# Optimization experiments

Hardware: AMD Instinct MI355X
Metric: run time of the kernel (lower is better)

The kernel has to match this reference:

```python
import jax, jax.numpy as jnp
import numpy as np

N = 100001      # item_num + 1
D = 64          # hidden_units
NNZ = 3200000   # number of nonzeros in encoder_adj (avg degree ~32)


def setup_inputs() -> dict:
    key = jax.random.key(0)
    k1, k2, k3, k4 = jax.random.split(key, 4)
    row_idx = jax.random.randint(k1, (NNZ,), 0, N, dtype=jnp.int32)
    col_idx = jax.random.randint(k2, (NNZ,), 0, N, dtype=jnp.int32)
    adj_vals = jax.random.uniform(k3, (NNZ,), dtype=jnp.float32)
    emb_weight = jax.random.normal(k4, (N, D), dtype=jnp.float32)
    return {"row_idx": row_idx, "col_idx": col_idx, "adj_vals": adj_vals,
            "emb_weight": emb_weight}


def _spmm(row_idx, col_idx, vals, x):
    # COO SpMM: out[r] += vals[e] * x[col[e]]  -> [N, D]
    gathered = vals[:, None] * x[col_idx]          # [NNZ, D]
    return jax.ops.segment_sum(gathered, row_idx, num_segments=N)


def reference(row_idx, col_idx, adj_vals, emb_weight):
    e0 = emb_weight                                 # ego embeddings
    e1 = _spmm(row_idx, col_idx, adj_vals, e0)      # GCN layer 1
    e2 = _spmm(row_idx, col_idx, adj_vals, e1)      # GCN layer 2
    summed = e0 + e1 + e2                           # sum(embeds)
    return (summed, e0, e1, e2)
```

## Files before the change

kernel.cpp:

```cpp
#include <hip/hip_runtime.h>
#include <stdint.h>

#define DHID 64
#define G_BLOCKS 1024
#define BMAX 1024
#define RPB 128

static inline size_t align256(size_t x) { return (x + 255) & ~(size_t)255; }


__global__ void zero_f32(float* __restrict__ p, size_t n) {
  size_t i = (size_t)blockIdx.x * blockDim.x + threadIdx.x;
  if (i < n) p[i] = 0.f;
}


__global__ __launch_bounds__(256) void
a1_hist_k(const int* __restrict__ row, int* __restrict__ histGB,
          int nnz, int B, int chunk) {
  __shared__ int h[BMAX];
  for (int i = threadIdx.x; i < B; i += 256) h[i] = 0;
  __syncthreads();
  int g = blockIdx.x;
  int s = g * chunk, e = min(nnz, s + chunk);
  int j = s + threadIdx.x;
  for (; j + 768 < e; j += 1024) {
    int r0 = row[j], r1 = row[j + 256], r2 = row[j + 512], r3 = row[j + 768];
    atomicAdd(&h[r0 >> 7], 1);
    atomicAdd(&h[r1 >> 7], 1);
    atomicAdd(&h[r2 >> 7], 1);
    atomicAdd(&h[r3 >> 7], 1);
  }
  for (; j < e; j += 256)
    atomicAdd(&h[row[j] >> 7], 1);
  __syncthreads();
  for (int i = threadIdx.x; i < B; i += 256)
    histGB[i * G_BLOCKS + g] = h[i];
}

__global__ __launch_bounds__(256) void
scan_gb_k(const int* __restrict__ histGB, int* __restrict__ offGB,
          int* __restrict__ btot, int B) {
  __shared__ int wsum[4];
  int b = blockIdx.x, t = threadIdx.x, lane = t & 63, w = t >> 6;
  int v[4];
  int s4 = 0;
#pragma unroll
  for (int i = 0; i < 4; ++i) {
    v[i] = histGB[b * G_BLOCKS + t * 4 + i];
    s4 += v[i];
  }
  int incl = s4;
#pragma unroll
  for (int off = 1; off < 64; off <<= 1) {
    int u = __shfl_up(incl, off);
    if (lane >= off) incl += u;
  }
  if (lane == 63) wsum[w] = incl;
  __syncthreads();
  int run = incl - s4;
  for (int w2 = 0; w2 < w; ++w2) run += wsum[w2];
#pragma unroll
  for (int i = 0; i < 4; ++i) {
    offGB[b * G_BLOCKS + t * 4 + i] = run;
    run += v[i];
  }
  if (t == 0) btot[b] = wsum[0] + wsum[1] + wsum[2] + wsum[3];
}

__global__ void scan_b_k(const int* __restrict__ btot, int* __restrict__ base, int B) {
  __shared__ int wsum[4];
  int t = threadIdx.x, lane = t & 63, w = t >> 6;
  int v[8];
  int s = 0;
#pragma unroll
  for (int i = 0; i < 8; ++i) {
    int idx = t * 8 + i;
    v[i] = (idx < B) ? btot[idx] : 0;
    s += v[i];
  }
  int incl = s;
#pragma unroll
  for (int off = 1; off < 64; off <<= 1) {
    int u = __shfl_up(incl, off);
    if (lane >= off) incl += u;
  }
  if (lane == 63) wsum[w] = incl;
  __syncthreads();
  int run = incl - s;
  for (int w2 = 0; w2 < w; ++w2) run += wsum[w2];
#pragma unroll
  for (int i = 0; i < 8; ++i) {
    int idx = t * 8 + i;
    if (idx <= B) base[idx] = run;
    run += v[i];
  }
}

__global__ __launch_bounds__(256) void
a2_scatter_k(const int* __restrict__ row, const int* __restrict__ col,
             const float* __restrict__ val, const int* __restrict__ base,
             const int* __restrict__ offGB, int2* __restrict__ stage,
             int nnz, int B, int chunk) {
  __shared__ int cur[BMAX];
  int g = blockIdx.x;
  for (int i = threadIdx.x; i < B; i += 256)
    cur[i] = base[i] + offGB[i * G_BLOCKS + g];
  __syncthreads();
  int s = g * chunk, e = min(nnz, s + chunk);
  int j = s + threadIdx.x;
  for (; j + 768 < e; j += 1024) {
    int r0 = row[j], r1 = row[j + 256], r2 = row[j + 512], r3 = row[j + 768];
    int c0 = col[j], c1 = col[j + 256], c2 = col[j + 512], c3 = col[j + 768];
    float v0 = val[j], v1 = val[j + 256], v2 = val[j + 512], v3 = val[j + 768];
    int p0 = atomicAdd(&cur[r0 >> 7], 1);
    int p1 = atomicAdd(&cur[r1 >> 7], 1);
    int p2 = atomicAdd(&cur[r2 >> 7], 1);
    int p3 = atomicAdd(&cur[r3 >> 7], 1);
    int2 q0; q0.x = ((r0 & 127) << 24) | c0; q0.y = __float_as_int(v0);
    int2 q1; q1.x = ((r1 & 127) << 24) | c1; q1.y = __float_as_int(v1);
    int2 q2; q2.x = ((r2 & 127) << 24) | c2; q2.y = __float_as_int(v2);
    int2 q3; q3.x = ((r3 & 127) << 24) | c3; q3.y = __float_as_int(v3);
    stage[p0] = q0;
    stage[p1] = q1;
    stage[p2] = q2;
    stage[p3] = q3;
  }
  for (; j < e; j += 256) {
    int r = row[j];
    int pos = atomicAdd(&cur[r >> 7], 1);
    int2 p;
    p.x = ((r & 127) << 24) | col[j];
    p.y = __float_as_int(val[j]);
    stage[pos] = p;
  }
}


__global__ __launch_bounds__(256) void
bgroup_k(const int* __restrict__ base, const int2* __restrict__ stage,
         int2* __restrict__ edges, int* __restrict__ rowstart, int n, int nnz) {
  __shared__ int h[RPB];
  __shared__ int cur[RPB];
  __shared__ int w0sum;
  int b = blockIdx.x, t = threadIdx.x;
  int lane = t & 63, w = t >> 6;
  if (t < RPB) h[t] = 0;
  __syncthreads();
  int s = base[b], e = base[b + 1];
  {
    int j = s + t;
    for (; j + 768 < e; j += 1024) {
      int a0 = ((unsigned)stage[j].x) >> 24;
      int a1 = ((unsigned)stage[j + 256].x) >> 24;
      int a2 = ((unsigned)stage[j + 512].x) >> 24;
      int a3 = ((unsigned)stage[j + 768].x) >> 24;
      atomicAdd(&h[a0], 1);
      atomicAdd(&h[a1], 1);
      atomicAdd(&h[a2], 1);
      atomicAdd(&h[a3], 1);
    }
    for (; j < e; j += 256)
      atomicAdd(&h[((unsigned)stage[j].x) >> 24], 1);
  }
  __syncthreads();
  int v = 0, incl = 0;
  if (t < RPB) {
    v = h[t];
    incl = v;
#pragma unroll
    for (int off = 1; off < 64; off <<= 1) {
      int u = __shfl_up(incl, off);
      if (lane >= off) incl += u;
    }
    if (t == 63) w0sum = incl;
  }
  __syncthreads();
  if (t < RPB) {
    int excl = incl - v + ((w == 1) ? w0sum : 0);
    cur[t] = s + excl;
    int r = (b << 7) + t;
    if (r < n) rowstart[r] = s + excl;
  }
  if (b == 0 && t == 0) rowstart[n] = nnz;
  __syncthreads();
  {
    int j = s + t;
    for (; j + 768 < e; j += 1024) {
      int2 p0 = stage[j], p1 = stage[j + 256], p2 = stage[j + 512], p3 = stage[j + 768];
      int q0 = atomicAdd(&cur[((unsigned)p0.x) >> 24], 1);
      int q1 = atomicAdd(&cur[((unsigned)p1.x) >> 24], 1);
      int q2 = atomicAdd(&cur[((unsigned)p2.x) >> 24], 1);
      int q3 = atomicAdd(&cur[((unsigned)p3.x) >> 24], 1);
      int2 o0; o0.x = p0.x & 0xFFFFFF; o0.y = p0.y;
      int2 o1; o1.x = p1.x & 0xFFFFFF; o1.y = p1.y;
      int2 o2; o2.x = p2.x & 0xFFFFFF; o2.y = p2.y;
      int2 o3; o3.x = p3.x & 0xFFFFFF; o3.y = p3.y;
      edges[q0] = o0;
      edges[q1] = o1;
      edges[q2] = o2;
      edges[q3] = o3;
    }
    for (; j < e; j += 256) {
      int2 p = stage[j];
      int pos = atomicAdd(&cur[((unsigned)p.x) >> 24], 1);
      int2 q;
      q.x = p.x & 0xFFFFFF;
      q.y = p.y;
      edges[pos] = q;
    }
  }
}


__global__ void spmm_k(const int* __restrict__ rowstart, const int2* __restrict__ edges,
                       const float* __restrict__ x, float* __restrict__ y, int n) {
  int wave = (blockIdx.x * blockDim.x + threadIdx.x) >> 6;
  int lane = threadIdx.x & 63;
  if (wave >= n) return;
  int start = __builtin_amdgcn_readfirstlane(rowstart[wave]);
  int end   = __builtin_amdgcn_readfirstlane(rowstart[wave + 1]);
  float acc = 0.f;
  int k = start;
  for (; k + 8 <= end; k += 8) {
    int2 e0 = edges[k + 0], e1 = edges[k + 1], e2 = edges[k + 2], e3 = edges[k + 3];
    int2 e4 = edges[k + 4], e5 = edges[k + 5], e6 = edges[k + 6], e7 = edges[k + 7];
    float x0 = x[((size_t)e0.x << 6) + lane];
    float x1 = x[((size_t)e1.x << 6) + lane];
    float x2 = x[((size_t)e2.x << 6) + lane];
    float x3 = x[((size_t)e3.x << 6) + lane];
    float x4 = x[((size_t)e4.x << 6) + lane];
    float x5 = x[((size_t)e5.x << 6) + lane];
    float x6 = x[((size_t)e6.x << 6) + lane];
    float x7 = x[((size_t)e7.x << 6) + lane];
    acc += __int_as_float(e0.y) * x0;
    acc += __int_as_float(e1.y) * x1;
    acc += __int_as_float(e2.y) * x2;
    acc += __int_as_float(e3.y) * x3;
    acc += __int_as_float(e4.y) * x4;
    acc += __int_as_float(e5.y) * x5;
    acc += __int_as_float(e6.y) * x6;
    acc += __int_as_float(e7.y) * x7;
  }
  for (; k < end; ++k) {
    int2 e = edges[k];
    acc += __int_as_float(e.y) * x[((size_t)e.x << 6) + lane];
  }
  y[((size_t)wave << 6) + lane] = acc;
}

__global__ void spmm_fused_k(const int* __restrict__ rowstart, const int2* __restrict__ edges,
                             const float* __restrict__ e0, const float* __restrict__ e1,
                             float* __restrict__ e2, float* __restrict__ summed,
                             float* __restrict__ e0out, int n) {
  int wave = (blockIdx.x * blockDim.x + threadIdx.x) >> 6;
  int lane = threadIdx.x & 63;
  if (wave >= n) return;
  int start = __builtin_amdgcn_readfirstlane(rowstart[wave]);
  int end   = __builtin_amdgcn_readfirstlane(rowstart[wave + 1]);
  float acc = 0.f;
  int k = start;
  for (; k + 8 <= end; k += 8) {
    int2 ea = edges[k + 0], eb = edges[k + 1], ec = edges[k + 2], ed = edges[k + 3];
    int2 ee = edges[k + 4], ef = edges[k + 5], eg = edges[k + 6], eh = edges[k + 7];
    float x0 = e1[((size_t)ea.x << 6) + lane];
    float x1 = e1[((size_t)eb.x << 6) + lane];
    float x2 = e1[((size_t)ec.x << 6) + lane];
    float x3 = e1[((size_t)ed.x << 6) + lane];
    float x4 = e1[((size_t)ee.x << 6) + lane];
    float x5 = e1[((size_t)ef.x << 6) + lane];
    float x6 = e1[((size_t)eg.x << 6) + lane];
    float x7 = e1[((size_t)eh.x << 6) + lane];
    acc += __int_as_float(ea.y) * x0;
    acc += __int_as_float(eb.y) * x1;
    acc += __int_as_float(ec.y) * x2;
    acc += __int_as_float(ed.y) * x3;
    acc += __int_as_float(ee.y) * x4;
    acc += __int_as_float(ef.y) * x5;
    acc += __int_as_float(eg.y) * x6;
    acc += __int_as_float(eh.y) * x7;
  }
  for (; k < end; ++k) {
    int2 e = edges[k];
    acc += __int_as_float(e.y) * e1[((size_t)e.x << 6) + lane];
  }
  size_t o = ((size_t)wave << 6) + lane;
  float v0 = e0[o];
  float v1 = e1[o];
  e2[o] = acc;
  summed[o] = v0 + v1 + acc;
  e0out[o] = v0;
}


__global__ void spmm_atomic_k(const int* __restrict__ row, const int* __restrict__ col,
                              const float* __restrict__ val, const float* __restrict__ x,
                              float* __restrict__ y, int nnz) {
  int wave = (blockIdx.x * blockDim.x + threadIdx.x) >> 6;
  int lane = threadIdx.x & 63;
  if (wave >= nnz) return;
  int r = row[wave]; int c = col[wave]; float v = val[wave];
  atomicAdd(&y[(size_t)r * DHID + lane], v * x[(size_t)c * DHID + lane]);
}

__global__ void sum_k(const float4* __restrict__ e0, const float4* __restrict__ e1,
                      const float4* __restrict__ e2, float4* __restrict__ summed,
                      float4* __restrict__ e0out, int n4) {
  int i = blockIdx.x * blockDim.x + threadIdx.x;
  if (i < n4) {
    float4 a = e0[i], b = e1[i], c = e2[i];
    float4 s;
    s.x = a.x + b.x + c.x;
    s.y = a.y + b.y + c.y;
    s.z = a.z + b.z + c.z;
    s.w = a.w + b.w + c.w;
    summed[i] = s;
    e0out[i] = a;
  }
}

extern "C" void kernel_launch(void* const* d_in, const int* in_sizes, int n_in,
                              void* d_out, int out_size, void* d_ws, size_t ws_size,
                              hipStream_t stream) {
  const int*   row = (const int*)d_in[0];
  const int*   col = (const int*)d_in[1];
  const float* val = (const float*)d_in[2];
  const float* emb = (const float*)d_in[3];
  int nnz = in_sizes[0];
  int n   = in_sizes[3] / DHID;
  size_t ND = (size_t)n * DHID;

  float* out    = (float*)d_out;
  float* summed = out;
  float* e0o    = out + ND;
  float* e1     = out + 2 * ND;
  float* e2     = out + 3 * ND;

  int B  = (n + RPB - 1) / RPB;
  int chunk = (nnz + G_BLOCKS - 1) / G_BLOCKS;

  size_t o0 = 0;
  size_t histGB_off   = o0; o0 += align256((size_t)B * G_BLOCKS * 4);
  size_t offGB_off    = o0; o0 += align256((size_t)B * G_BLOCKS * 4);
  size_t btot_off     = o0; o0 += align256((size_t)B * 4);
  size_t base_off     = o0; o0 += align256((size_t)(B + 1) * 4);
  size_t rowstart_off = o0; o0 += align256((size_t)(n + 1) * 4);
  size_t stage_off    = o0; o0 += align256((size_t)nnz * 8);
  size_t edges_off    = o0; o0 += align256((size_t)nnz * 8);
  size_t need_sorted = o0;

  bool use_sorted = (ws_size >= need_sorted) && (B <= BMAX) && (n < (1 << 24));

  int rb = (int)((ND + 255) / 256);
  int n4 = (int)(ND / 4);
  int sb = (n4 + 255) / 256;
  int wb = (int)(((size_t)nnz * 64 + 255) / 256);

  if (use_sorted) {
    uint8_t* w = (uint8_t*)d_ws;
    int*  histGB   = (int*)(w + histGB_off);
    int*  offGB    = (int*)(w + offGB_off);
    int*  btot     = (int*)(w + btot_off);
    int*  base     = (int*)(w + base_off);
    int*  rowstart = (int*)(w + rowstart_off);
    int2* stage    = (int2*)(w + stage_off);
    int2* edges    = (int2*)(w + edges_off);

    a1_hist_k<<<G_BLOCKS, 256, 0, stream>>>(row, histGB, nnz, B, chunk);
    scan_gb_k<<<B, 256, 0, stream>>>(histGB, offGB, btot, B);
    scan_b_k<<<1, 256, 0, stream>>>(btot, base, B);
    a2_scatter_k<<<G_BLOCKS, 256, 0, stream>>>(row, col, val, base, offGB, stage,
                                               nnz, B, chunk);
    bgroup_k<<<B, 256, 0, stream>>>(base, stage, edges, rowstart, n, nnz);

    spmm_k<<<rb, 256, 0, stream>>>(rowstart, edges, emb, e1, n);
    spmm_fused_k<<<rb, 256, 0, stream>>>(rowstart, edges, emb, e1, e2, summed, e0o, n);
  } else {
    zero_f32<<<(int)((ND + 255) / 256), 256, 0, stream>>>(e1, ND);
    spmm_atomic_k<<<wb, 256, 0, stream>>>(row, col, val, emb, e1, nnz);
    zero_f32<<<(int)((ND + 255) / 256), 256, 0, stream>>>(e2, ND);
    spmm_atomic_k<<<wb, 256, 0, stream>>>(row, col, val, e1, e2, nnz);
    sum_k<<<sb, 256, 0, stream>>>((const float4*)emb, (const float4*)e1,
                                  (const float4*)e2, (float4*)summed,
                                  (float4*)e0o, n4);
  }
}
```

Before: 433.1 us.

## Fuse per-bucket row grouping into SpMM kernels using LDS edge buffer

Removes the separate bgroup kernel that wrote a fully row-sorted edge array and rowstart to global memory. Each SpMM block now loads its bucket of 128 rows from the staging array, counting-sorts the edges by row in shared memory (up to 4608 edges), then computes the rows from LDS. This saves a global write and re-read of the edge list and one launch. In exchange the sort runs twice (once per layer), only 782 blocks of 512 threads run with a large LDS footprint, and a slow fallback path handles buckets that overflow the buffer.

New measurement: 432.6 us. No clear change (-0.1%).

```diff
diff --git a/kernel.cpp b/kernel.cpp
--- a/kernel.cpp
+++ b/kernel.cpp
@@ -5,6 +5,7 @@
 #define G_BLOCKS 1024
 #define BMAX 1024
 #define RPB 128
+#define CAP 4608
 
 static inline size_t align256(size_t x) { return (x + 255) & ~(size_t)255; }
 
@@ -137,159 +138,200 @@
 }
 
 
-__global__ __launch_bounds__(256) void
-bgroup_k(const int* __restrict__ base, const int2* __restrict__ stage,
-         int2* __restrict__ edges, int* __restrict__ rowstart, int n, int nnz) {
-  __shared__ int h[RPB];
-  __shared__ int cur[RPB];
+__global__ __launch_bounds__(512) void
+spmm_csr_k(const int* __restrict__ base, const int2* __restrict__ stage,
+           const float* __restrict__ x, float* __restrict__ y, int n) {
+  __shared__ int2 ebuf[CAP];
+  __shared__ int h[RPB], rowoff[RPB], cur[RPB];
   __shared__ int w0sum;
   int b = blockIdx.x, t = threadIdx.x;
   int lane = t & 63, w = t >> 6;
   if (t < RPB) h[t] = 0;
   __syncthreads();
-  int s = base[b], e = base[b + 1];
-  {
-    int j = s + t;
-    for (; j + 768 < e; j += 1024) {
-      int a0 = ((unsigned)stage[j].x) >> 24;
-      int a1 = ((unsigned)stage[j + 256].x) >> 24;
-      int a2 = ((unsigned)stage[j + 512].x) >> 24;
-      int a3 = ((unsigned)stage[j + 768].x) >> 24;
-      atomicAdd(&h[a0], 1);
-      atomicAdd(&h[a1], 1);
-      atomicAdd(&h[a2], 1);
-      atomicAdd(&h[a3], 1);
-    }
-    for (; j < e; j += 256)
+  int s = __builtin_amdgcn_readfirstlane(base[b]);
+  int e = __builtin_amdgcn_readfirstlane(base[b + 1]);
+  int cnt = e - s;
+  if (cnt <= CAP) {
+    for (int j = s + t; j < e; j += 512)
       atomicAdd(&h[((unsigned)stage[j].x) >> 24], 1);
-  }
-  __syncthreads();
-  int v = 0, incl = 0;
-  if (t < RPB) {
-    v = h[t];
-    incl = v;
-#pragma unroll
-    for (int off = 1; off < 64; off <<= 1) {
-      int u = __shfl_up(incl, off);
-      if (lane >= off) incl += u;
-    }
-    if (t == 63) w0sum = incl;
-  }
-  __syncthreads();
-  if (t < RPB) {
-    int excl = incl - v + ((w == 1) ? w0sum : 0);
-    cur[t] = s + excl;
-    int r = (b << 7) + t;
-    if (r < n) rowstart[r] = s + excl;
-  }
-  if (b == 0 && t == 0) rowstart[n] = nnz;
-  __syncthreads();
-  {
-    int j = s + t;
-    for (; j + 768 < e; j += 1024) {
-      int2 p0 = stage[j], p1 = stage[j + 256], p2 = stage[j + 512], p3 = stage[j + 768];
-      int q0 = atomicAdd(&cur[((unsigned)p0.x) >> 24], 1);
-      int q1 = atomicAdd(&cur[((unsigned)p1.x) >> 24], 1);
-      int q2 = atomicAdd(&cur[((unsigned)p2.x) >> 24], 1);
-      int q3 = atomicAdd(&cur[((unsigned)p3.x) >> 24], 1);
-      int2 o0; o0.x = p0.x & 0xFFFFFF; o0.y = p0.y;
-      int2 o1; o1.x = p1.x & 0xFFFFFF; o1.y = p1.y;
-      int2 o2; o2.x = p2.x & 0xFFFFFF; o2.y = p2.y;
-      int2 o3; o3.x = p3.x & 0xFFFFFF; o3.y = p3.y;
-      edges[q0] = o0;
-      edges[q1] = o1;
-      edges[q2] = o2;
-      edges[q3] = o3;
-    }
-    for (; j < e; j += 256) {
+    __syncthreads();
+    int v = 0, part = 0;
+    if (t < RPB) {
+      v = h[t];
+      int incl = v;
+#pragma unroll
+      for (int off = 1; off < 64; off <<= 1) {
+        int u = __shfl_up(incl, off);
+        if (lane >= off) incl += u;
+      }
+      if (t == 63) w0sum = incl;
+      part = incl - v;
+    }
+    __syncthreads();
+    if (t < RPB) {
+      int excl = part + ((t >= 64) ? w0sum : 0);
+      rowoff[t] = excl;
+      cur[t] = excl;
+    }
+    __syncthreads();
+    for (int j = s + t; j < e; j += 512) {
       int2 p = stage[j];
-      int pos = atomicAdd(&cur[((unsigned)p.x) >> 24], 1);
-      int2 q;
-      q.x = p.x & 0xFFFFFF;
-      q.y = p.y;
-      edges[pos] = q;
-    }
-  }
-}
-
-
-__global__ void spmm_k(const int* __restrict__ rowstart, const int2* __restrict__ edges,
-                       const float* __restrict__ x, float* __restrict__ y, int n) {
-  int wave = (blockIdx.x * blockDim.x + threadIdx.x) >> 6;
-  int lane = threadIdx.x & 63;
-  if (wave >= n) return;
-  int start = __builtin_amdgcn_readfirstlane(rowstart[wave]);
-  int end   = __builtin_amdgcn_readfirstlane(rowstart[wave + 1]);
-  float acc = 0.f;
-  int k = start;
-  for (; k + 8 <= end; k += 8) {
-    int2 e0 = edges[k + 0], e1 = edges[k + 1], e2 = edges[k + 2], e3 = edges[k + 3];
-    int2 e4 = edges[k + 4], e5 = edges[k + 5], e6 = edges[k + 6], e7 = edges[k + 7];
-    float x0 = x[((size_t)e0.x << 6) + lane];
-    float x1 = x[((size_t)e1.x << 6) + lane];
-    float x2 = x[((size_t)e2.x << 6) + lane];
-    float x3 = x[((size_t)e3.x << 6) + lane];
-    float x4 = x[((size_t)e4.x << 6) + lane];
-    float x5 = x[((size_t)e5.x << 6) + lane];
-    float x6 = x[((size_t)e6.x << 6) + lane];
-    float x7 = x[((size_t)e7.x << 6) + lane];
-    acc += __int_as_float(e0.y) * x0;
-    acc += __int_as_float(e1.y) * x1;
-    acc += __int_as_float(e2.y) * x2;
-    acc += __int_as_float(e3.y) * x3;
-    acc += __int_as_float(e4.y) * x4;
-    acc += __int_as_float(e5.y) * x5;
-    acc += __int_as_float(e6.y) * x6;
-    acc += __int_as_float(e7.y) * x7;
-  }
-  for (; k < end; ++k) {
-    int2 e = edges[k];
-    acc += __int_as_float(e.y) * x[((size_t)e.x << 6) + lane];
-  }
-  y[((size_t)wave << 6) + lane] = acc;
-}
-
-__global__ void spmm_fused_k(const int* __restrict__ rowstart, const int2* __restrict__ edges,
-                             const float* __restrict__ e0, const float* __restrict__ e1,
-                             float* __restrict__ e2, float* __restrict__ summed,
-                             float* __restrict__ e0out, int n) {
-  int wave = (blockIdx.x * blockDim.x + threadIdx.x) >> 6;
-  int lane = threadIdx.x & 63;
-  if (wave >= n) return;
-  int start = __builtin_amdgcn_readfirstlane(rowstart[wave]);
-  int end   = __builtin_amdgcn_readfirstlane(rowstart[wave + 1]);
-  float acc = 0.f;
-  int k = start;
-  for (; k + 8 <= end; k += 8) {
-    int2 ea = edges[k + 0], eb = edges[k + 1], ec = edges[k + 2], ed = edges[k + 3];
-    int2 ee = edges[k + 4], ef = edges[k + 5], eg = edges[k + 6], eh = edges[k + 7];
-    float x0 = e1[((size_t)ea.x << 6) + lane];
-    float x1 = e1[((size_t)eb.x << 6) + lane];
-    float x2 = e1[((size_t)ec.x << 6) + lane];
-    float x3 = e1[((size_t)ed.x << 6) + lane];
-    float x4 = e1[((size_t)ee.x << 6) + lane];
-    float x5 = e1[((size_t)ef.x << 6) + lane];
-    float x6 = e1[((size_t)eg.x << 6) + lane];
-    float x7 = e1[((size_t)eh.x << 6) + lane];
-    acc += __int_as_float(ea.y) * x0;
-    acc += __int_as_float(eb.y) * x1;
-    acc += __int_as_float(ec.y) * x2;
-    acc += __int_as_float(ed.y) * x3;
-    acc += __int_as_float(ee.y) * x4;
-    acc += __int_as_float(ef.y) * x5;
-    acc += __int_as_float(eg.y) * x6;
-    acc += __int_as_float(eh.y) * x7;
-  }
-  for (; k < end; ++k) {
-    int2 e = edges[k];
-    acc += __int_as_float(e.y) * e1[((size_t)e.x << 6) + lane];
-  }
-  size_t o = ((size_t)wave << 6) + lane;
-  float v0 = e0[o];
-  float v1 = e1[o];
-  e2[o] = acc;
-  summed[o] = v0 + v1 + acc;
-  e0out[o] = v0;
+      int r = ((unsigned)p.x) >> 24;
+      int pos = atomicAdd(&cur[r], 1);
+      int2 q; q.x = p.x & 0xFFFFFF; q.y = p.y;
+      ebuf[pos] = q;
+    }
+    __syncthreads();
+    for (int rr = w * 16; rr < w * 16 + 16; ++rr) {
+      int R = (b << 7) + rr;
+      if (R >= n) continue;
+      int start = __builtin_amdgcn_readfirstlane(rowoff[rr]);
+      int end   = __builtin_amdgcn_readfirstlane(cur[rr]);
+      float acc = 0.f;
+      int k = start;
+      for (; k + 8 <= end; k += 8) {
+        int2 e0 = ebuf[k + 0], e1 = ebuf[k + 1], e2 = ebuf[k + 2], e3 = ebuf[k + 3];
+        int2 e4 = ebuf[k + 4], e5 = ebuf[k + 5], e6 = ebuf[k + 6], e7 = ebuf[k + 7];
+        float x0 = x[((size_t)e0.x << 6) + lane];
+        float x1 = x[((size_t)e1.x << 6) + lane];
+        float x2 = x[((size_t)e2.x << 6) + lane];
+        float x3 = x[((size_t)e3.x << 6) + lane];
+        float x4 = x[((size_t)e4.x << 6) + lane];
+        float x5 = x[((size_t)e5.x << 6) + lane];
+        float x6 = x[((size_t)e6.x << 6) + lane];
+        float x7 = x[((size_t)e7.x << 6) + lane];
+        acc += __int_as_float(e0.y) * x0;
+        acc += __int_as_float(e1.y) * x1;
+        acc += __int_as_float(e2.y) * x2;
+        acc += __int_as_float(e3.y) * x3;
+        acc += __int_as_float(e4.y) * x4;
+        acc += __int_as_float(e5.y) * x5;
+        acc += __int_as_float(e6.y) * x6;
+        acc += __int_as_float(e7.y) * x7;
+      }
+      for (; k < end; ++k) {
+        int2 p = ebuf[k];
+        acc += __int_as_float(p.y) * x[((size_t)p.x << 6) + lane];
+      }
+      y[((size_t)R << 6) + lane] = acc;
+    }
+  } else {
+    for (int rr = w * 16; rr < w * 16 + 16; ++rr) {
+      int R = (b << 7) + rr;
+      if (R >= n) continue;
+      float acc = 0.f;
+      for (int j = s; j < e; ++j) {
+        int2 p = stage[j];
+        if ((int)(((unsigned)p.x) >> 24) == rr)
+          acc += __int_as_float(p.y) * x[((size_t)(p.x & 0xFFFFFF) << 6) + lane];
+      }
+      y[((size_t)R << 6) + lane] = acc;
+    }
+  }
+}
+
+__global__ __launch_bounds__(512) void
+spmm_csr_fused_k(const int* __restrict__ base, const int2* __restrict__ stage,
+                 const float* __restrict__ e0g, const float* __restrict__ e1g,
+                 float* __restrict__ e2g, float* __restrict__ summed,
+                 float* __restrict__ e0out, int n) {
+  __shared__ int2 ebuf[CAP];
+  __shared__ int h[RPB], rowoff[RPB], cur[RPB];
+  __shared__ int w0sum;
+  int b = blockIdx.x, t = threadIdx.x;
+  int lane = t & 63, w = t >> 6;
+  if (t < RPB) h[t] = 0;
+  __syncthreads();
+  int s = __builtin_amdgcn_readfirstlane(base[b]);
+  int e = __builtin_amdgcn_readfirstlane(base[b + 1]);
+  int cnt = e - s;
+  if (cnt <= CAP) {
+    for (int j = s + t; j < e; j += 512)
+      atomicAdd(&h[((unsigned)stage[j].x) >> 24], 1);
+    __syncthreads();
+    int v = 0, part = 0;
+    if (t < RPB) {
+      v = h[t];
+      int incl = v;
+#pragma unroll
+      for (int off = 1; off < 64; off <<= 1) {
+        int u = __shfl_up(incl, off);
+        if (lane >= off) incl += u;
+      }
+      if (t == 63) w0sum = incl;
+      part = incl - v;
+    }
+    __syncthreads();
+    if (t < RPB) {
+      int excl = part + ((t >= 64) ? w0sum : 0);
+      rowoff[t] = excl;
+      cur[t] = excl;
+    }
+    __syncthreads();
+    for (int j = s + t; j < e; j += 512) {
+      int2 p = stage[j];
+      int r = ((unsigned)p.x) >> 24;
+      int pos = atomicAdd(&cur[r], 1);
+      int2 q; q.x = p.x & 0xFFFFFF; q.y = p.y;
+      ebuf[pos] = q;
+    }
+    __syncthreads();
+    for (int rr = w * 16; rr < w * 16 + 16; ++rr) {
+      int R = (b << 7) + rr;
+      if (R >= n) continue;
+      int start = __builtin_amdgcn_readfirstlane(rowoff[rr]);
+      int end   = __builtin_amdgcn_readfirstlane(cur[rr]);
+      float acc = 0.f;
+      int k = start;
+      for (; k + 8 <= end; k += 8) {
+        int2 ea = ebuf[k + 0], eb = ebuf[k + 1], ec = ebuf[k + 2], ed = ebuf[k + 3];
+        int2 ee = ebuf[k + 4], ef = ebuf[k + 5], eg = ebuf[k + 6], eh = ebuf[k + 7];
+        float x0 = e1g[((size_t)ea.x << 6) + lane];
+        float x1 = e1g[((size_t)eb.x << 6) + lane];
+        float x2 = e1g[((size_t)ec.x << 6) + lane];
+        float x3 = e1g[((size_t)ed.x << 6) + lane];
+        float x4 = e1g[((size_t)ee.x << 6) + lane];
+        float x5 = e1g[((size_t)ef.x << 6) + lane];
+        float x6 = e1g[((size_t)eg.x << 6) + lane];
+        float x7 = e1g[((size_t)eh.x << 6) + lane];
+        acc += __int_as_float(ea.y) * x0;
+        acc += __int_as_float(eb.y) * x1;
+        acc += __int_as_float(ec.y) * x2;
+        acc += __int_as_float(ed.y) * x3;
+        acc += __int_as_float(ee.y) * x4;
+        acc += __int_as_float(ef.y) * x5;
+        acc += __int_as_float(eg.y) * x6;
+        acc += __int_as_float(eh.y) * x7;
+      }
+      for (; k < end; ++k) {
+        int2 p = ebuf[k];
+        acc += __int_as_float(p.y) * e1g[((size_t)p.x << 6) + lane];
+      }
+      size_t o = ((size_t)R << 6) + lane;
+      float v0 = e0g[o];
+      float v1 = e1g[o];
+      e2g[o] = acc;
+      summed[o] = v0 + v1 + acc;
+      e0out[o] = v0;
+    }
+  } else {
+    for (int rr = w * 16; rr < w * 16 + 16; ++rr) {
+      int R = (b << 7) + rr;
+      if (R >= n) continue;
+      float acc = 0.f;
+      for (int j = s; j < e; ++j) {
+        int2 p = stage[j];
+        if ((int)(((unsigned)p.x) >> 24) == rr)
+          acc += __int_as_float(p.y) * e1g[((size_t)(p.x & 0xFFFFFF) << 6) + lane];
+      }
+      size_t o = ((size_t)R << 6) + lane;
+      float v0 = e0g[o];
+      float v1 = e1g[o];
+      e2g[o] = acc;
+      summed[o] = v0 + v1 + acc;
+      e0out[o] = v0;
+    }
+  }
 }
 
 
@@ -340,41 +382,35 @@
   int chunk = (nnz + G_BLOCKS - 1) / G_BLOCKS;
 
   size_t o0 = 0;
-  size_t histGB_off   = o0; o0 += align256((size_t)B * G_BLOCKS * 4);
-  size_t offGB_off    = o0; o0 += align256((size_t)B * G_BLOCKS * 4);
-  size_t btot_off     = o0; o0 += align256((size_t)B * 4);
-  size_t base_off     = o0; o0 += align256((size_t)(B + 1) * 4);
-  size_t rowstart_off = o0; o0 += align256((size_t)(n + 1) * 4);
-  size_t stage_off    = o0; o0 += align256((size_t)nnz * 8);
-  size_t edges_off    = o0; o0 += align256((size_t)nnz * 8);
+  size_t histGB_off = o0; o0 += align256((size_t)B * G_BLOCKS * 4);
+  size_t offGB_off  = o0; o0 += align256((size_t)B * G_BLOCKS * 4);
+  size_t btot_off   = o0; o0 += align256((size_t)B * 4);
+  size_t base_off   = o0; o0 += align256((size_t)(B + 1) * 4);
+  size_t stage_off  = o0; o0 += align256((size_t)nnz * 8);
   size_t need_sorted = o0;
 
   bool use_sorted = (ws_size >= need_sorted) && (B <= BMAX) && (n < (1 << 24));
 
-  int rb = (int)((ND + 255) / 256);
   int n4 = (int)(ND / 4);
   int sb = (n4 + 255) / 256;
   int wb = (int)(((size_t)nnz * 64 + 255) / 256);
 
   if (use_sorted) {
     uint8_t* w = (uint8_t*)d_ws;
-    int*  histGB   = (int*)(w + histGB_off);
-    int*  offGB    = (int*)(w + offGB_off);
-    int*  btot     = (int*)(w + btot_off);
-    int*  base     = (int*)(w + base_off);
-    int*  rowstart = (int*)(w + rowstart_off);
-    int2* stage    = (int2*)(w + stage_off);
-    int2* edges    = (int2*)(w + edges_off);
+    int*  histGB = (int*)(w + histGB_off);
+    int*  offGB  = (int*)(w + offGB_off);
+    int*  btot   = (int*)(w + btot_off);
+    int*  base   = (int*)(w + base_off);
+    int2* stage  = (int2*)(w + stage_off);
 
     a1_hist_k<<<G_BLOCKS, 256, 0, stream>>>(row, histGB, nnz, B, chunk);
     scan_gb_k<<<B, 256, 0, stream>>>(histGB, offGB, btot, B);
     scan_b_k<<<1, 256, 0, stream>>>(btot, base, B);
     a2_scatter_k<<<G_BLOCKS, 256, 0, stream>>>(row, col, val, base, offGB, stage,
                                                nnz, B, chunk);
-    bgroup_k<<<B, 256, 0, stream>>>(base, stage, edges, rowstart, n, nnz);
-
-    spmm_k<<<rb, 256, 0, stream>>>(rowstart, edges, emb, e1, n);
-    spmm_fused_k<<<rb, 256, 0, stream>>>(rowstart, edges, emb, e1, e2, summed, e0o, n);
+
+    spmm_csr_k<<<B, 512, 0, stream>>>(base, stage, emb, e1, n);
+    spmm_csr_fused_k<<<B, 512, 0, stream>>>(base, stage, emb, e1, e2, summed, e0o, n);
   } else {
     zero_f32<<<(int)((ND + 255) / 256), 256, 0, stream>>>(e1, ND);
     spmm_atomic_k<<<wb, 256, 0, stream>>>(row, col, val, emb, e1, nnz);
```
